# Optimization experiments

Measured on AMD Instinct MI355X. Metric: run time of the kernel, lower is better.

## Reference

```python
import jax, jax.numpy as jnp
import numpy as np

NUM_HEADS = 8
HEAD_DIM = 16


def setup_inputs() -> dict:
    key = jax.random.key(0)
    ks = jax.random.split(key, 9)
    B, S, E, H = 2, 4096, 16, 128
    sc_in = 1.0 / np.sqrt(E)
    sc_h = 1.0 / np.sqrt(H)
    return {
        "x": jax.random.normal(ks[0], (B, S, E), dtype=jnp.float32),
        "wq": jax.random.normal(ks[1], (H, E), dtype=jnp.float32) * sc_in,
        "bq": jax.random.normal(ks[2], (H,), dtype=jnp.float32) * 0.02,
        "wk": jax.random.normal(ks[3], (H, E), dtype=jnp.float32) * sc_in,
        "bk": jax.random.normal(ks[4], (H,), dtype=jnp.float32) * 0.02,
        "wv": jax.random.normal(ks[5], (H, E), dtype=jnp.float32) * sc_in,
        "bv": jax.random.normal(ks[6], (H,), dtype=jnp.float32) * 0.02,
        "wo": jax.random.normal(ks[7], (E, H), dtype=jnp.float32) * sc_h,
        "bo": jax.random.normal(ks[8], (E,), dtype=jnp.float32) * 0.02,
    }


def reference(x, wq, bq, wk, bk, wv, bv, wo, bo):
    B, S, E = x.shape
    H = wq.shape[0]
    nh, hd = NUM_HEADS, HEAD_DIM
    # QKV projections (torch Linear: y = x @ W.T + b)
    q = x @ wq.T + bq  # [B,S,H]
    k = x @ wk.T + bk
    v = x @ wv.T + bv
    # split heads -> [B,nh,S,hd]
    q = q.reshape(B, S, nh, hd).transpose(0, 2, 1, 3)
    k = k.reshape(B, S, nh, hd).transpose(0, 2, 1, 3)
    v = v.reshape(B, S, nh, hd).transpose(0, 2, 1, 3)
    # flex_attention with block_mask=None == full SDPA, scale = 1/sqrt(head_dim)
    scale = 1.0 / np.sqrt(hd)
    scores = jnp.einsum("bhqd,bhkd->bhqk", q, k) * scale  # [B,nh,S,S]
    attn = jax.nn.softmax(scores, axis=-1)
    out = jnp.einsum("bhqk,bhkd->bhqd", attn, v)  # [B,nh,S,hd]
    out = out.transpose(0, 2, 1, 3).reshape(B, S, H)
    return out @ wo.T + bo
```

## Files before the change

### kernel.cpp

```cpp
#include <hip/hip_runtime.h>
#include <hip/hip_bf16.h>
#include <math.h>

#define NH 8
#define HD 16
#define EE 16
#define HH 128
#define NCH 4
#define QR 16

typedef __attribute__((ext_vector_type(8)))  short short8;
typedef __attribute__((ext_vector_type(16))) float f32x16;
typedef __attribute__((ext_vector_type(4)))  float f32x4;

#define EXP2F(x) __builtin_amdgcn_exp2f(x)

__global__ __launch_bounds__(256) void qkv_fused(
        const float* __restrict__ x,
        const float* __restrict__ wq, const float* __restrict__ bq,
        const float* __restrict__ wk, const float* __restrict__ bk,
        const float* __restrict__ wv, const float* __restrict__ bv,
        __hip_bfloat16* __restrict__ Qb, __hip_bfloat16* __restrict__ Kb,
        __hip_bfloat16* __restrict__ Vt, float* __restrict__ OutZero, int S) {
    int row0 = blockIdx.x * QR;
    int b = row0 / S, s0 = row0 - b * S;
    int tid = threadIdx.x;

    OutZero[(size_t)blockIdx.x * 256 + tid] = 0.f;

    __shared__ __align__(16) float xs[QR][EE];
    __shared__ __align__(16) short qsb[QR][136];
    __shared__ __align__(16) short ksb[QR][136];
    __shared__ __align__(16) short vsb[QR][136];

    ((float*)xs)[tid] = x[(size_t)row0 * EE + tid];
    __syncthreads();

    int h = tid & 127, sub = tid >> 7;
    float wqr[16], wkr[16], wvr[16];
    const float4* wq4 = (const float4*)(wq + h * EE);
    const float4* wk4 = (const float4*)(wk + h * EE);
    const float4* wv4 = (const float4*)(wv + h * EE);
#pragma unroll
    for (int j = 0; j < 4; ++j) {
        float4 a = wq4[j]; wqr[4*j]=a.x; wqr[4*j+1]=a.y; wqr[4*j+2]=a.z; wqr[4*j+3]=a.w;
        float4 c = wk4[j]; wkr[4*j]=c.x; wkr[4*j+1]=c.y; wkr[4*j+2]=c.z; wkr[4*j+3]=c.w;
        float4 d = wv4[j]; wvr[4*j]=d.x; wvr[4*j+1]=d.y; wvr[4*j+2]=d.z; wvr[4*j+3]=d.w;
    }
    float bqv = bq[h], bkv = bk[h], bvv = bv[h];

#pragma unroll
    for (int rr = 0; rr < 8; ++rr) {
        int r = (sub << 3) + rr;
        const float4* xv = (const float4*)xs[r];
        float aq = bqv, ak = bkv, av = bvv;
#pragma unroll
        for (int j = 0; j < 4; ++j) {
            float4 xe = xv[j];
            aq += xe.x*wqr[4*j] + xe.y*wqr[4*j+1] + xe.z*wqr[4*j+2] + xe.w*wqr[4*j+3];
            ak += xe.x*wkr[4*j] + xe.y*wkr[4*j+1] + xe.z*wkr[4*j+2] + xe.w*wkr[4*j+3];
            av += xe.x*wvr[4*j] + xe.y*wvr[4*j+1] + xe.z*wvr[4*j+2] + xe.w*wvr[4*j+3];
        }
        __hip_bfloat16 qb = __float2bfloat16(aq * 0.36067376022f);
        __hip_bfloat16 kb = __float2bfloat16(ak);
        __hip_bfloat16 vb = __float2bfloat16(av);
        qsb[r][h] = *reinterpret_cast<short*>(&qb);
        ksb[r][h] = *reinterpret_cast<short*>(&kb);
        vsb[r][h] = *reinterpret_cast<short*>(&vb);
    }
    __syncthreads();

    {
        int pr = tid & 127;
        int r = pr & 15, head = pr >> 4;
        if (tid < 128) {
            short8 a = *(const short8*)&qsb[r][head * 16];
            short8 c = *(const short8*)&qsb[r][head * 16 + 8];
            short* dst = (short*)Qb + ((size_t)(b * NH + head) * S + s0 + r) * HD;
            *(short8*)dst = a;
            *(short8*)(dst + 8) = c;
        } else {
            short8 a = *(const short8*)&ksb[r][head * 16];
            short8 c = *(const short8*)&ksb[r][head * 16 + 8];
            short* dst = (short*)Kb + ((size_t)(b * NH + head) * S + s0 + r) * HD;
            *(short8*)dst = a;
            *(short8*)(dst + 8) = c;
        }
    }
    {
        int hd_idx = tid >> 1;
        int head2 = hd_idx >> 4, d2 = hd_idx & 15;
        int si0 = (tid & 1) * 8;
        short8 w0;
#pragma unroll
        for (int j = 0; j < 8; ++j) w0[j] = vsb[si0 + j][hd_idx];
        short* dst = (short*)Vt + ((size_t)(b * NH + head2) * HD + d2) * S + s0 + si0;
        *(short8*)dst = w0;
    }
}

__global__ __launch_bounds__(256, 8) void attn(const __hip_bfloat16* __restrict__ Qb,
                                               const __hip_bfloat16* __restrict__ Kb,
                                               const __hip_bfloat16* __restrict__ Vtb,
                                               const float* __restrict__ wo,
                                               const float* __restrict__ bo,
                                               float* __restrict__ Out,
                                               int S, int BH) {
    int blk = blockIdx.x;
    int bh = blk & (16 - 1);
    int q0 = (blk >> 4) * 32;
    int cb = threadIdx.x >> 6;
    int lane = threadIdx.x & 63;
    int ql = lane & 31, half = lane >> 5;
    int l15 = lane & 15, l4 = lane >> 4;
    int CS = S / NCH;
    int kbeg = cb * CS;

    __shared__ __align__(16) union {
        short pt[NCH][32 * 40];
        struct { float o[NCH][32][16]; float l[NCH][32]; } red;
    } sm;
    __shared__ __align__(16) float onorm[32][16];
    short* pt = sm.pt[cb];

    const short* qptr = (const short*)Qb + ((size_t)bh * S + q0) * HD;
    const short* kf_ptr = (const short*)Kb + ((size_t)bh * S + kbeg + ql) * HD + 8 * half;
    const short* vf_ptr = (const short*)Vtb + ((size_t)bh * HD + l15) * S + kbeg + 8 * l4;

    short8 qf = *(const short8*)(qptr + ql * HD + 8 * half);

    short8 ones8;
#pragma unroll
    for (int j = 0; j < 8; ++j) ones8[j] = (short)0x3F80;

    f32x16 zc;
#pragma unroll
    for (int i = 0; i < 16; ++i) zc[i] = 0.f;

    f32x4 o0, o1, ol0, ol1;
#pragma unroll
    for (int i = 0; i < 4; ++i) { o0[i] = 0.f; o1[i] = 0.f; ol0[i] = 0.f; ol1[i] = 0.f; }

    int wswz = ((ql >> 3) & 3) << 3;
    int rswz0 = ((l15 >> 3) & 3) << 3;
    int rswz1 = (((l15 + 16) >> 3) & 3) << 3;

    short8 kf = *(const short8*)kf_ptr;
    short8 vf = *(const short8*)vf_ptr;

    for (int it = 0; it < CS / 32; ++it) {
        kf_ptr += 32 * HD;
        vf_ptr += 32;
        short8 kf_n = *(const short8*)kf_ptr;
        short8 vf_n = *(const short8*)vf_ptr;

        f32x16 st = __builtin_amdgcn_mfma_f32_32x32x16_bf16(kf, qf, zc, 0, 0, 0);

        float pf[16];
#pragma unroll
        for (int r = 0; r < 16; ++r) pf[r] = EXP2F(st[r]);

        union PU { __hip_bfloat162 b2; unsigned u; };
        unsigned pk[8];
#pragma unroll
        for (int i = 0; i < 8; ++i) {
            float2 f2; f2.x = pf[2 * i]; f2.y = pf[2 * i + 1];
            PU pu; pu.b2 = __float22bfloat162_rn(f2);
            pk[i] = pu.u;
        }
#pragma unroll
        for (int i = 0; i < 4; ++i) {
            uint2 w; w.x = pk[2 * i]; w.y = pk[2 * i + 1];
            *(uint2*)&pt[ql * 40 + ((8 * i + 4 * half) ^ wswz)] = w;
        }
        short8 p0 = *(const short8*)&pt[l15 * 40 + ((8 * l4) ^ rswz0)];
        short8 p1 = *(const short8*)&pt[(l15 + 16) * 40 + ((8 * l4) ^ rswz1)];

        o0 = __builtin_amdgcn_mfma_f32_16x16x32_bf16(vf, p0, o0, 0, 0, 0);
        o1 = __builtin_amdgcn_mfma_f32_16x16x32_bf16(vf, p1, o1, 0, 0, 0);
        ol0 = __builtin_amdgcn_mfma_f32_16x16x32_bf16(ones8, p0, ol0, 0, 0, 0);
        ol1 = __builtin_amdgcn_mfma_f32_16x16x32_bf16(ones8, p1, ol1, 0, 0, 0);

        kf = kf_n;
        vf = vf_n;
    }

    __syncthreads();
    {
        float4 r0; r0.x = o0[0]; r0.y = o0[1]; r0.z = o0[2]; r0.w = o0[3];
        float4 r1; r1.x = o1[0]; r1.y = o1[1]; r1.z = o1[2]; r1.w = o1[3];
        *(float4*)&sm.red.o[cb][l15][4 * l4]      = r0;
        *(float4*)&sm.red.o[cb][l15 + 16][4 * l4] = r1;
        if (l4 == 0) {
            sm.red.l[cb][l15]      = ol0[0];
            sm.red.l[cb][l15 + 16] = ol1[0];
        }
    }
    __syncthreads();

    if (threadIdx.x < 128) {
        int q = threadIdx.x >> 2, quad = threadIdx.x & 3;
        float4 acc; acc.x = 0.f; acc.y = 0.f; acc.z = 0.f; acc.w = 0.f;
        float ls = 0.f;
#pragma unroll
        for (int c = 0; c < NCH; ++c) {
            float4 v = *(const float4*)&sm.red.o[c][q][4 * quad];
            acc.x += v.x; acc.y += v.y; acc.z += v.z; acc.w += v.w;
            ls += sm.red.l[c][q];
        }
        float inv = 1.f / ls;
        acc.x *= inv; acc.y *= inv; acc.z *= inv; acc.w *= inv;
        *(float4*)&onorm[q][4 * quad] = acc;
    }
    __syncthreads();

    int b = bh >> 3, head = bh & 7;
#pragma unroll
    for (int i = 0; i < 2; ++i) {
        int p = threadIdx.x + 256 * i;
        int q = p >> 4, e = p & 15;
        const float4* w4 = (const float4*)(wo + e * HH + head * HD);
        const float4* o4 = (const float4*)&onorm[q][0];
        float acc = bo[e] * (1.0f / NH);
#pragma unroll
        for (int j = 0; j < 4; ++j) {
            float4 w = w4[j];
            float4 o = o4[j];
            acc += w.x * o.x + w.y * o.y + w.z * o.z + w.w * o.w;
        }
        atomicAdd(&Out[((size_t)(b * S + q0 + q)) * EE + e], acc);
    }
}

extern "C" void kernel_launch(void* const* d_in, const int* in_sizes, int n_in,
                              void* d_out, int out_size, void* d_ws, size_t ws_size,
                              hipStream_t stream) {
    const float* x  = (const float*)d_in[0];
    const float* wq = (const float*)d_in[1];
    const float* bq = (const float*)d_in[2];
    const float* wk = (const float*)d_in[3];
    const float* bk = (const float*)d_in[4];
    const float* wv = (const float*)d_in[5];
    const float* bv = (const float*)d_in[6];
    const float* wo = (const float*)d_in[7];
    const float* bo = (const float*)d_in[8];
    float* out = (float*)d_out;

    int rows = in_sizes[0] / EE;
    int S = 4096;
    int B = rows / S;
    int BH = B * NH;

    size_t n = (size_t)rows * HH;
    __hip_bfloat16* Qb = (__hip_bfloat16*)d_ws;
    __hip_bfloat16* Kb = Qb + n;
    __hip_bfloat16* Vt = Kb + n;

    qkv_fused<<<rows / QR, 256, 0, stream>>>(x, wq, bq, wk, bk, wv, bv, Qb, Kb, Vt, out, S);
    attn<<<(S / 32) * BH, 256, 0, stream>>>(Qb, Kb, Vt, wo, bo, out, S, BH);
}
```

Measured before the change: 122.1 us.

## Keep softmax probabilities in registers using 16x16x32 MFMA layout, drop LDS staging

The attention inner loop switches from one 32x32x16 QK MFMA, which needed P written to and re-read from LDS to transpose it into the PV operand layout, to 16x16x32 MFMAs. Their output layout packs directly into the B operand of the PV MFMA, so P stays in registers. Q is zero-padded in the K dimension to fit the 32-deep MFMA, and V loads become two 4-element reads per lane. This removes per-iteration LDS traffic and the separate prefetch, at the cost of twice the QK MFMA work (half of it on zero padding) and a lower occupancy hint in launch bounds.

Measured after the change: 156.6 us. 28.3% more time.

```diff
diff --git a/kernel.cpp b/kernel.cpp
--- a/kernel.cpp
+++ b/kernel.cpp
@@ -10,10 +10,11 @@
 #define QR 16
 
 typedef __attribute__((ext_vector_type(8)))  short short8;
-typedef __attribute__((ext_vector_type(16))) float f32x16;
+typedef __attribute__((ext_vector_type(4)))  short s16x4;
 typedef __attribute__((ext_vector_type(4)))  float f32x4;
 
 #define EXP2F(x) __builtin_amdgcn_exp2f(x)
+#define MFMA32(a, b, c) __builtin_amdgcn_mfma_f32_16x16x32_bf16((a), (b), (c), 0, 0, 0)
 
 __global__ __launch_bounds__(256) void qkv_fused(
         const float* __restrict__ x,
@@ -99,7 +100,7 @@
     }
 }
 
-__global__ __launch_bounds__(256, 8) void attn(const __hip_bfloat16* __restrict__ Qb,
+__global__ __launch_bounds__(256, 6) void attn(const __hip_bfloat16* __restrict__ Qb,
                                                const __hip_bfloat16* __restrict__ Kb,
                                                const __hip_bfloat16* __restrict__ Vtb,
                                                const float* __restrict__ wo,
@@ -111,89 +112,77 @@
     int q0 = (blk >> 4) * 32;
     int cb = threadIdx.x >> 6;
     int lane = threadIdx.x & 63;
-    int ql = lane & 31, half = lane >> 5;
     int l15 = lane & 15, l4 = lane >> 4;
     int CS = S / NCH;
     int kbeg = cb * CS;
 
-    __shared__ __align__(16) union {
-        short pt[NCH][32 * 40];
-        struct { float o[NCH][32][16]; float l[NCH][32]; } red;
-    } sm;
+    __shared__ __align__(16) struct { float o[NCH][32][16]; float l[NCH][32]; } red;
     __shared__ __align__(16) float onorm[32][16];
-    short* pt = sm.pt[cb];
-
-    const short* qptr = (const short*)Qb + ((size_t)bh * S + q0) * HD;
-    const short* kf_ptr = (const short*)Kb + ((size_t)bh * S + kbeg + ql) * HD + 8 * half;
-    const short* vf_ptr = (const short*)Vtb + ((size_t)bh * HD + l15) * S + kbeg + 8 * l4;
-
-    short8 qf = *(const short8*)(qptr + ql * HD + 8 * half);
+
+    short8 qf0, qf1;
+#pragma unroll
+    for (int j = 0; j < 8; ++j) { qf0[j] = 0; qf1[j] = 0; }
+    if (l4 < 2) {
+        const short* qbase = (const short*)Qb + ((size_t)bh * S + q0) * HD + 8 * l4;
+        qf0 = *(const short8*)(qbase + l15 * HD);
+        qf1 = *(const short8*)(qbase + (l15 + 16) * HD);
+    }
+
+    const short* kptr = (const short*)Kb + ((size_t)bh * S + kbeg + l15) * HD + 8 * (l4 & 1);
+    const short* vptr = (const short*)Vtb + ((size_t)bh * HD + l15) * S + kbeg + 4 * l4;
 
     short8 ones8;
 #pragma unroll
     for (int j = 0; j < 8; ++j) ones8[j] = (short)0x3F80;
 
-    f32x16 zc;
-#pragma unroll
-    for (int i = 0; i < 16; ++i) zc[i] = 0.f;
-
-    f32x4 o0, o1, ol0, ol1;
-#pragma unroll
-    for (int i = 0; i < 4; ++i) { o0[i] = 0.f; o1[i] = 0.f; ol0[i] = 0.f; ol1[i] = 0.f; }
-
-    int wswz = ((ql >> 3) & 3) << 3;
-    int rswz0 = ((l15 >> 3) & 3) << 3;
-    int rswz1 = (((l15 + 16) >> 3) & 3) << 3;
-
-    short8 kf = *(const short8*)kf_ptr;
-    short8 vf = *(const short8*)vf_ptr;
-
-    for (int it = 0; it < CS / 32; ++it) {
-        kf_ptr += 32 * HD;
-        vf_ptr += 32;
-        short8 kf_n = *(const short8*)kf_ptr;
-        short8 vf_n = *(const short8*)vf_ptr;
-
-        f32x16 st = __builtin_amdgcn_mfma_f32_32x32x16_bf16(kf, qf, zc, 0, 0, 0);
-
-        float pf[16];
-#pragma unroll
-        for (int r = 0; r < 16; ++r) pf[r] = EXP2F(st[r]);
-
-        union PU { __hip_bfloat162 b2; unsigned u; };
-        unsigned pk[8];
-#pragma unroll
-        for (int i = 0; i < 8; ++i) {
-            float2 f2; f2.x = pf[2 * i]; f2.y = pf[2 * i + 1];
-            PU pu; pu.b2 = __float22bfloat162_rn(f2);
-            pk[i] = pu.u;
-        }
-#pragma unroll
-        for (int i = 0; i < 4; ++i) {
-            uint2 w; w.x = pk[2 * i]; w.y = pk[2 * i + 1];
-            *(uint2*)&pt[ql * 40 + ((8 * i + 4 * half) ^ wswz)] = w;
-        }
-        short8 p0 = *(const short8*)&pt[l15 * 40 + ((8 * l4) ^ rswz0)];
-        short8 p1 = *(const short8*)&pt[(l15 + 16) * 40 + ((8 * l4) ^ rswz1)];
-
-        o0 = __builtin_amdgcn_mfma_f32_16x16x32_bf16(vf, p0, o0, 0, 0, 0);
-        o1 = __builtin_amdgcn_mfma_f32_16x16x32_bf16(vf, p1, o1, 0, 0, 0);
-        ol0 = __builtin_amdgcn_mfma_f32_16x16x32_bf16(ones8, p0, ol0, 0, 0, 0);
-        ol1 = __builtin_amdgcn_mfma_f32_16x16x32_bf16(ones8, p1, ol1, 0, 0, 0);
-
-        kf = kf_n;
-        vf = vf_n;
-    }
-
-    __syncthreads();
+    f32x4 zero4;
+#pragma unroll
+    for (int i = 0; i < 4; ++i) zero4[i] = 0.f;
+
+    f32x4 o0 = zero4, o1 = zero4, ol0 = zero4, ol1 = zero4;
+
+    int NIT = CS / 32;
+    for (int it = 0; it < NIT; ++it) {
+        short8 k0 = *(const short8*)kptr;
+        short8 k1 = *(const short8*)(kptr + 16 * HD);
+        s16x4 v0 = *(const s16x4*)vptr;
+        s16x4 v1 = *(const s16x4*)(vptr + 16);
+        kptr += 32 * HD;
+        vptr += 32;
+
+        union VU { s16x4 h[2]; short8 s8; } vu;
+        vu.h[0] = v0; vu.h[1] = v1;
+
+        f32x4 sa = MFMA32(k0, qf0, zero4);
+        f32x4 sb = MFMA32(k1, qf0, zero4);
+        union PU { __hip_bfloat162 h2[4]; short8 s8; } u0;
+        float2 a;
+        a.x = EXP2F(sa[0]); a.y = EXP2F(sa[1]); u0.h2[0] = __float22bfloat162_rn(a);
+        a.x = EXP2F(sa[2]); a.y = EXP2F(sa[3]); u0.h2[1] = __float22bfloat162_rn(a);
+        a.x = EXP2F(sb[0]); a.y = EXP2F(sb[1]); u0.h2[2] = __float22bfloat162_rn(a);
+        a.x = EXP2F(sb[2]); a.y = EXP2F(sb[3]); u0.h2[3] = __float22bfloat162_rn(a);
+        o0  = MFMA32(vu.s8,  u0.s8, o0);
+        ol0 = MFMA32(ones8, u0.s8, ol0);
+
+        f32x4 sc = MFMA32(k0, qf1, zero4);
+        f32x4 sd = MFMA32(k1, qf1, zero4);
+        union PU u1;
+        a.x = EXP2F(sc[0]); a.y = EXP2F(sc[1]); u1.h2[0] = __float22bfloat162_rn(a);
+        a.x = EXP2F(sc[2]); a.y = EXP2F(sc[3]); u1.h2[1] = __float22bfloat162_rn(a);
+        a.x = EXP2F(sd[0]); a.y = EXP2F(sd[1]); u1.h2[2] = __float22bfloat162_rn(a);
+        a.x = EXP2F(sd[2]); a.y = EXP2F(sd[3]); u1.h2[3] = __float22bfloat162_rn(a);
+        o1  = MFMA32(vu.s8,  u1.s8, o1);
+        ol1 = MFMA32(ones8, u1.s8, ol1);
+    }
+
     {
         float4 r0; r0.x = o0[0]; r0.y = o0[1]; r0.z = o0[2]; r0.w = o0[3];
         float4 r1; r1.x = o1[0]; r1.y = o1[1]; r1.z = o1[2]; r1.w = o1[3];
-        *(float4*)&sm.red.o[cb][l15][4 * l4]      = r0;
-        *(float4*)&sm.red.o[cb][l15 + 16][4 * l4] = r1;
+        *(float4*)&red.o[cb][l15][4 * l4]      = r0;
+        *(float4*)&red.o[cb][l15 + 16][4 * l4] = r1;
         if (l4 == 0) {
-            sm.red.l[cb][l15]      = ol0[0];
-            sm.red.l[cb][l15 + 16] = ol1[0];
+            red.l[cb][l15]      = ol0[0];
+            red.l[cb][l15 + 16] = ol1[0];
         }
     }
     __syncthreads();
@@ -204,9 +193,9 @@
         float ls = 0.f;
 #pragma unroll
         for (int c = 0; c < NCH; ++c) {
-            float4 v = *(const float4*)&sm.red.o[c][q][4 * quad];
+            float4 v = *(const float4*)&red.o[c][q][4 * quad];
             acc.x += v.x; acc.y += v.y; acc.z += v.z; acc.w += v.w;
-            ls += sm.red.l[c][q];
+            ls += red.l[c][q];
         }
         float inv = 1.f / ls;
         acc.x *= inv; acc.y *= inv; acc.z *= inv; acc.w *= inv;
```

## Software-pipeline attention loop with double-buffered P tile in LDS

Applied to the files above, without the earlier changes.

Restructures the key loop into a two-stage software pipeline. Each iteration computes QK^T and the exp/pack for the current tile into one LDS buffer, while the PV and row-sum MFMAs consume the previous tile from the other buffer. It also raises wave priority around the PV MFMAs. The aim is to overlap exp VALU work with MFMA and hide LDS write-read latency, at the cost of double the LDS per wave, which may reduce occupancy at 8 blocks per CU. There is also a prologue/epilogue. No barrier is needed, since each wave uses its own buffers.

New measurement: 133.1 us. 1.09x slower.

```diff
diff --git a/kernel.cpp b/kernel.cpp
--- a/kernel.cpp
+++ b/kernel.cpp
@@ -117,11 +117,12 @@
     int kbeg = cb * CS;
 
     __shared__ __align__(16) union {
-        short pt[NCH][32 * 40];
+        short pt[NCH][2][32 * 40];
         struct { float o[NCH][32][16]; float l[NCH][32]; } red;
     } sm;
     __shared__ __align__(16) float onorm[32][16];
-    short* pt = sm.pt[cb];
+    short* pt0 = sm.pt[cb][0];
+    short* pt1 = sm.pt[cb][1];
 
     const short* qptr = (const short*)Qb + ((size_t)bh * S + q0) * HD;
     const short* kf_ptr = (const short*)Kb + ((size_t)bh * S + kbeg + ql) * HD + 8 * half;
@@ -145,21 +146,10 @@
     int rswz0 = ((l15 >> 3) & 3) << 3;
     int rswz1 = (((l15 + 16) >> 3) & 3) << 3;
 
-    short8 kf = *(const short8*)kf_ptr;
-    short8 vf = *(const short8*)vf_ptr;
-
-    for (int it = 0; it < CS / 32; ++it) {
-        kf_ptr += 32 * HD;
-        vf_ptr += 32;
-        short8 kf_n = *(const short8*)kf_ptr;
-        short8 vf_n = *(const short8*)vf_ptr;
-
-        f32x16 st = __builtin_amdgcn_mfma_f32_32x32x16_bf16(kf, qf, zc, 0, 0, 0);
-
+    auto exppack = [&](const f32x16& st, short* ptw) {
         float pf[16];
 #pragma unroll
         for (int r = 0; r < 16; ++r) pf[r] = EXP2F(st[r]);
-
         union PU { __hip_bfloat162 b2; unsigned u; };
         unsigned pk[8];
 #pragma unroll
@@ -171,18 +161,53 @@
 #pragma unroll
         for (int i = 0; i < 4; ++i) {
             uint2 w; w.x = pk[2 * i]; w.y = pk[2 * i + 1];
-            *(uint2*)&pt[ql * 40 + ((8 * i + 4 * half) ^ wswz)] = w;
-        }
-        short8 p0 = *(const short8*)&pt[l15 * 40 + ((8 * l4) ^ rswz0)];
-        short8 p1 = *(const short8*)&pt[(l15 + 16) * 40 + ((8 * l4) ^ rswz1)];
-
-        o0 = __builtin_amdgcn_mfma_f32_16x16x32_bf16(vf, p0, o0, 0, 0, 0);
-        o1 = __builtin_amdgcn_mfma_f32_16x16x32_bf16(vf, p1, o1, 0, 0, 0);
-        ol0 = __builtin_amdgcn_mfma_f32_16x16x32_bf16(ones8, p0, ol0, 0, 0, 0);
-        ol1 = __builtin_amdgcn_mfma_f32_16x16x32_bf16(ones8, p1, ol1, 0, 0, 0);
-
-        kf = kf_n;
-        vf = vf_n;
+            *(uint2*)&ptw[ql * 40 + ((8 * i + 4 * half) ^ wswz)] = w;
+        }
+    };
+
+    short8 kf = *(const short8*)kf_ptr;
+    short8 vf_cur = *(const short8*)vf_ptr;
+    {
+        f32x16 st = __builtin_amdgcn_mfma_f32_32x32x16_bf16(kf, qf, zc, 0, 0, 0);
+        exppack(st, pt0);
+    }
+    kf_ptr += 32 * HD; kf = *(const short8*)kf_ptr;
+    short8 vf_prev = vf_cur;
+    vf_ptr += 32; vf_cur = *(const short8*)vf_ptr;
+
+    int NIT = CS / 32;
+#pragma unroll 2
+    for (int it = 1; it < NIT; ++it) {
+        short* ptw = (it & 1) ? pt1 : pt0;
+        const short* ptr_prev = (it & 1) ? pt0 : pt1;
+
+        f32x16 st = __builtin_amdgcn_mfma_f32_32x32x16_bf16(kf, qf, zc, 0, 0, 0);
+
+        short8 p0 = *(const short8*)&ptr_prev[l15 * 40 + ((8 * l4) ^ rswz0)];
+        short8 p1 = *(const short8*)&ptr_prev[(l15 + 16) * 40 + ((8 * l4) ^ rswz1)];
+
+        exppack(st, ptw);
+
+        __builtin_amdgcn_s_setprio(1);
+        o0  = __builtin_amdgcn_mfma_f32_16x16x32_bf16(vf_prev, p0, o0, 0, 0, 0);
+        o1  = __builtin_amdgcn_mfma_f32_16x16x32_bf16(vf_prev, p1, o1, 0, 0, 0);
+        ol0 = __builtin_amdgcn_mfma_f32_16x16x32_bf16(ones8,   p0, ol0, 0, 0, 0);
+        ol1 = __builtin_amdgcn_mfma_f32_16x16x32_bf16(ones8,   p1, ol1, 0, 0, 0);
+        __builtin_amdgcn_s_setprio(0);
+
+        kf_ptr += 32 * HD; kf = *(const short8*)kf_ptr;
+        vf_prev = vf_cur;
+        vf_ptr += 32; vf_cur = *(const short8*)vf_ptr;
+    }
+
+    {
+        const short* ptr_prev = ((NIT - 1) & 1) ? pt1 : pt0;
+        short8 p0 = *(const short8*)&ptr_prev[l15 * 40 + ((8 * l4) ^ rswz0)];
+        short8 p1 = *(const short8*)&ptr_prev[(l15 + 16) * 40 + ((8 * l4) ^ rswz1)];
+        o0  = __builtin_amdgcn_mfma_f32_16x16x32_bf16(vf_prev, p0, o0, 0, 0, 0);
+        o1  = __builtin_amdgcn_mfma_f32_16x16x32_bf16(vf_prev, p1, o1, 0, 0, 0);
+        ol0 = __builtin_amdgcn_mfma_f32_16x16x32_bf16(ones8,   p0, ol0, 0, 0, 0);
+        ol1 = __builtin_amdgcn_mfma_f32_16x16x32_bf16(ones8,   p1, ol1, 0, 0, 0);
     }
 
     __syncthreads();
```
